# Performance work log

Measured on AMD Instinct MI355X. Metric: run time of the kernel, lower is better.

Reference implementation:

```python
import jax, jax.numpy as jnp
import numpy as np

D_MODEL = 128
N_HEADS = 4
D_K = D_V = 32
LN_EPS = 1e-5


def setup_inputs() -> dict:
    key = jax.random.key(0)
    ks = jax.random.split(key, 12)
    B, S = 8, 2048
    scale = 1.0 / np.sqrt(D_MODEL)
    inp = {
        "Q": jax.random.normal(ks[0], (B, S, D_MODEL), jnp.float32),
        "K": jax.random.normal(ks[1], (B, S, D_MODEL), jnp.float32),
        "V": jax.random.normal(ks[2], (B, S, D_MODEL), jnp.float32),
        "attn_mask": jnp.zeros((B, S, S), jnp.bool_),
        # learned params (torch Linear stored as [in, out] so y = x @ W + b)
        "wq": jax.random.normal(ks[3], (D_MODEL, N_HEADS * D_K), jnp.float32) * scale,
        "bq": jnp.zeros((N_HEADS * D_K,), jnp.float32),
        "wk": jax.random.normal(ks[4], (D_MODEL, N_HEADS * D_K), jnp.float32) * scale,
        "bk": jnp.zeros((N_HEADS * D_K,), jnp.float32),
        "wv": jax.random.normal(ks[5], (D_MODEL, N_HEADS * D_V), jnp.float32) * scale,
        "bv": jnp.zeros((N_HEADS * D_V,), jnp.float32),
        "wo": jax.random.normal(ks[6], (N_HEADS * D_V, D_MODEL), jnp.float32) * scale,
        "bo": jnp.zeros((D_MODEL,), jnp.float32),
        "gamma": jnp.ones((D_MODEL,), jnp.float32),
        "beta": jnp.zeros((D_MODEL,), jnp.float32),
    }
    return inp


def _layer_norm(x, gamma, beta):
    mu = jnp.mean(x, axis=-1, keepdims=True)
    var = jnp.mean(jnp.square(x - mu), axis=-1, keepdims=True)
    return (x - mu) * jax.lax.rsqrt(var + LN_EPS) * gamma + beta


def reference(Q, K, V, attn_mask, wq, bq, wk, bk, wv, bv, wo, bo, gamma, beta):
    B, S, _ = Q.shape
    residual = Q
    # project and split heads: [B, H, S, Dk]
    q = (Q @ wq + bq).reshape(B, S, N_HEADS, D_K).transpose(0, 2, 1, 3)
    k = (K @ wk + bk).reshape(B, S, N_HEADS, D_K).transpose(0, 2, 1, 3)
    v = (V @ wv + bv).reshape(B, S, N_HEADS, D_V).transpose(0, 2, 1, 3)
    scores = jnp.einsum("bhqd,bhkd->bhqk", q, k) / np.sqrt(D_K)
    scores = jnp.where(attn_mask[:, None, :, :], -1e9, scores)
    attn = jax.nn.softmax(scores, axis=-1)
    context = jnp.einsum("bhqk,bhkd->bhqd", attn, v)
    context = context.transpose(0, 2, 1, 3).reshape(B, S, N_HEADS * D_V)
    output = context @ wo + bo
    out = _layer_norm(output + residual, gamma, beta)
    return out, attn
```

## Files before the change

kernel.cpp:

```cpp
#include <hip/hip_runtime.h>

typedef _Float16 f16;
typedef __attribute__((ext_vector_type(8))) _Float16 f16x8;
typedef __attribute__((ext_vector_type(4))) _Float16 f16x4;
typedef __attribute__((ext_vector_type(2))) __fp16 fp16x2;
typedef __attribute__((ext_vector_type(4))) float f32x4;
typedef unsigned int u32;
typedef __attribute__((ext_vector_type(2))) unsigned int u32x2;
typedef __attribute__((ext_vector_type(4))) unsigned int u32x4;

#define S_LEN 2048
#define NB 8
#define NH 4
#define DM 128
#define DK 32

static __device__ __forceinline__ f32x4 mfma_16x16x32(f16x8 a, f16x8 b, f32x4 c) {
  return __builtin_amdgcn_mfma_f32_16x16x32_f16(a, b, c, 0, 0, 0);
}
static __device__ __forceinline__ float exp2f_fast(float x) {
  return __builtin_amdgcn_exp2f(x);
}

union H8 { f16x8 v; fp16x2 h[4]; };
union H4 { f16x4 v; fp16x2 h[2]; };

__global__ __launch_bounds__(256) void pack_mask_kernel(
    const unsigned char* __restrict__ mask, u32* __restrict__ words)
{
  const int tid = blockIdx.x * 256 + threadIdx.x;
  u32x4 v = *(const u32x4*)(mask + (size_t)tid * 16);
  u32 bits = 0;
#pragma unroll
  for (int i = 0; i < 4; ++i) {
    u32 u = v[i];
#pragma unroll
    for (int k = 0; k < 4; ++k)
      bits |= (((u >> (8 * k)) & 0xffu) ? 1u : 0u) << (4 * i + k);
  }
  u32 other = __shfl_xor(bits, 1);
  if ((threadIdx.x & 1) == 0) words[tid >> 1] = bits | (other << 16);
}

__global__ __launch_bounds__(256) void proj_kernel(
    const float* __restrict__ Qx, const float* __restrict__ Kx, const float* __restrict__ Vx,
    const float* __restrict__ wq, const float* __restrict__ bq,
    const float* __restrict__ wk, const float* __restrict__ bk,
    const float* __restrict__ wv, const float* __restrict__ bv,
    f16* __restrict__ qh, f16* __restrict__ kh, f16* __restrict__ vt)
{
  const int mode = blockIdx.y;
  const float* X = (mode == 0) ? Qx : (mode == 1) ? Kx : Vx;
  const float* W = (mode == 0) ? wq : (mode == 1) ? wk : wv;
  const float* Bp = (mode == 0) ? bq : (mode == 1) ? bk : bv;

  __shared__ f16 wl[128 * 136];
#pragma unroll
  for (int i = 0; i < 16; ++i) {
    int idx = (i * 256 + threadIdx.x) * 4;
    int k = idx >> 7, j = idx & 127;
    f32x4 w4 = *(const f32x4*)(W + idx);
    wl[(j    ) * 136 + k] = (f16)w4[0];
    wl[(j + 1) * 136 + k] = (f16)w4[1];
    wl[(j + 2) * 136 + k] = (f16)w4[2];
    wl[(j + 3) * 136 + k] = (f16)w4[3];
  }
  __syncthreads();

  const int wave = threadIdx.x >> 6, lane = threadIdx.x & 63;
  const int ln = lane & 15, hi = lane >> 4;
  const int rows0 = blockIdx.x * 64 + wave * 16;
  const int b = rows0 >> 11;
  const int s0 = rows0 & (S_LEN - 1);

  f32x4 acc[8];
#pragma unroll
  for (int jg = 0; jg < 8; ++jg) acc[jg] = (f32x4){0.f, 0.f, 0.f, 0.f};

#pragma unroll
  for (int kc = 0; kc < 4; ++kc) {
    const float* xp = X + (size_t)(rows0 + ln) * DM + kc * 32 + hi * 8;
    f32x4 x0 = *(const f32x4*)xp;
    f32x4 x1 = *(const f32x4*)(xp + 4);
    H8 hx;
    hx.h[0] = __builtin_amdgcn_cvt_pkrtz(x0[0], x0[1]);
    hx.h[1] = __builtin_amdgcn_cvt_pkrtz(x0[2], x0[3]);
    hx.h[2] = __builtin_amdgcn_cvt_pkrtz(x1[0], x1[1]);
    hx.h[3] = __builtin_amdgcn_cvt_pkrtz(x1[2], x1[3]);
    const f16* wp = wl + ln * 136 + kc * 32 + hi * 8;
    if (mode < 2) {
#pragma unroll
      for (int jg = 0; jg < 8; ++jg) {
        f16x8 wf = *(const f16x8*)(wp + jg * 2176);
        acc[jg] = mfma_16x16x32(wf, hx.v, acc[jg]);
      }
    } else {
#pragma unroll
      for (int jg = 0; jg < 8; ++jg) {
        f16x8 wf = *(const f16x8*)(wp + jg * 2176);
        acc[jg] = mfma_16x16x32(hx.v, wf, acc[jg]);
      }
    }
  }

  if (mode < 2) {
    const float sc = (mode == 0) ? 0.25503531f : 1.0f;
    f16* outp = (mode == 0) ? qh : kh;
    const int s = s0 + ln;
#pragma unroll
    for (int jg = 0; jg < 8; ++jg) {
      int j0 = jg * 16 + hi * 4;
      f32x4 bb = *(const f32x4*)(Bp + j0);
      int h = jg >> 1;
      int dd0 = (jg & 1) * 16 + hi * 4;
      f16x4 e;
#pragma unroll
      for (int r = 0; r < 4; ++r) e[r] = (f16)((acc[jg][r] + bb[r]) * sc);
      *(f16x4*)(outp + ((size_t)(b * NH + h) * S_LEN + s) * DK + dd0) = e;
    }
  } else {
    const int t4 = s0 >> 5;
    const int halfq = (s0 >> 4) & 1;
#pragma unroll
    for (int jt = 0; jt < 8; ++jt) {
      int h = jt >> 1;
      int dv = (jt & 1) * 16 + ln;
      float bb = Bp[jt * 16 + ln];
      H4 u;
      u.h[0] = __builtin_amdgcn_cvt_pkrtz(acc[jt][0] + bb, acc[jt][1] + bb);
      u.h[1] = __builtin_amdgcn_cvt_pkrtz(acc[jt][2] + bb, acc[jt][3] + bb);
      f16* dst = vt + (size_t)(b * NH + h) * DK * S_LEN + t4 * 1024 + dv * 32 + hi * 8 + halfq * 4;
      *(f16x4*)dst = u.v;
    }
  }
}

__global__ __launch_bounds__(256, 4) void attn_kernel(
    const f16* __restrict__ qh, const f16* __restrict__ kh, const f16* __restrict__ vt,
    const u32* __restrict__ words,
    float* __restrict__ attn, float* __restrict__ ctx)
{
  const int bx = blockIdx.x;
  const int bh = bx >> 5;
  const int qp = bx & 31;
  const int wave = threadIdx.x >> 6;
  const int tile = wave >> 1;
  const int half = wave & 1;
  const int lane = threadIdx.x & 63;
  const int ln = lane & 15, hi = lane >> 4;
  const int b = bh >> 2, h = bh & 3;
  const int base = qp * 64 + tile * 32;
  const int rA = base + ln;
  const int rB = rA + 16;
  const int kv0 = half * (S_LEN / 2);

  __shared__ f32x4 pt[4][2][16][16];
  __shared__ float sums[2][2][2][16];

  const f16* kbase = kh + (size_t)bh * S_LEN * DK;
  const f16* vbase = vt + (size_t)bh * DK * S_LEN;
  const u32* wrA = words + ((size_t)b * S_LEN + rA) * (S_LEN / 32);
  const u32* wrB = words + ((size_t)b * S_LEN + rB) * (S_LEN / 32);

  const f16x8 qA = *(const f16x8*)(qh + ((size_t)bh * S_LEN + rA) * DK + hi * 8);
  const f16x8 qB = *(const f16x8*)(qh + ((size_t)bh * S_LEN + rB) * DK + hi * 8);
  const f32x4 zero = {0.f, 0.f, 0.f, 0.f};

  float smA = 0.f, smB = 0.f;
  {
    const f16* kp = kbase + (size_t)(kv0 + ln) * DK + hi * 8;
    const u32* mpA = wrA + (kv0 >> 5);
    const u32* mpB = wrB + (kv0 >> 5);
    f16x8 k0 = *(const f16x8*)(kp);
    f16x8 k1 = *(const f16x8*)(kp + 512);
    f16x8 k2 = *(const f16x8*)(kp + 1024);
    f16x8 k3 = *(const f16x8*)(kp + 1536);
    u32x2 mA = *(const u32x2*)mpA;
    u32x2 mB = *(const u32x2*)mpB;
    for (int it = 0; it < 16; ++it) {
      f16x8 n0, n1, n2, n3;
      u32x2 nA, nB;
      if (it < 15) {
        n0 = *(const f16x8*)(kp + 2048);
        n1 = *(const f16x8*)(kp + 2560);
        n2 = *(const f16x8*)(kp + 3072);
        n3 = *(const f16x8*)(kp + 3584);
        nA = *(const u32x2*)(mpA + 2);
        nB = *(const u32x2*)(mpB + 2);
      }
      f32x4 sA0 = mfma_16x16x32(k0, qA, zero);
      f32x4 sA1 = mfma_16x16x32(k1, qA, zero);
      f32x4 sA2 = mfma_16x16x32(k2, qA, zero);
      f32x4 sA3 = mfma_16x16x32(k3, qA, zero);
      f32x4 sB0 = mfma_16x16x32(k0, qB, zero);
      f32x4 sB1 = mfma_16x16x32(k1, qB, zero);
      f32x4 sB2 = mfma_16x16x32(k2, qB, zero);
      f32x4 sB3 = mfma_16x16x32(k3, qB, zero);
      if (__any(((mA[0] | mA[1]) | (mB[0] | mB[1])) != 0u)) {
#pragma unroll
        for (int r = 0; r < 4; ++r) {
          float a0 = ((mA[0] >> (4 * hi + r)) & 1) ? 0.f : exp2f_fast(sA0[r]);
          float a1 = ((mA[0] >> (16 + 4 * hi + r)) & 1) ? 0.f : exp2f_fast(sA1[r]);
          float a2 = ((mA[1] >> (4 * hi + r)) & 1) ? 0.f : exp2f_fast(sA2[r]);
          float a3 = ((mA[1] >> (16 + 4 * hi + r)) & 1) ? 0.f : exp2f_fast(sA3[r]);
          smA += (a0 + a1) + (a2 + a3);
          float b0 = ((mB[0] >> (4 * hi + r)) & 1) ? 0.f : exp2f_fast(sB0[r]);
          float b1 = ((mB[0] >> (16 + 4 * hi + r)) & 1) ? 0.f : exp2f_fast(sB1[r]);
          float b2 = ((mB[1] >> (4 * hi + r)) & 1) ? 0.f : exp2f_fast(sB2[r]);
          float b3 = ((mB[1] >> (16 + 4 * hi + r)) & 1) ? 0.f : exp2f_fast(sB3[r]);
          smB += (b0 + b1) + (b2 + b3);
        }
      } else {
#pragma unroll
        for (int r = 0; r < 4; ++r) {
          smA += (exp2f_fast(sA0[r]) + exp2f_fast(sA1[r])) + (exp2f_fast(sA2[r]) + exp2f_fast(sA3[r]));
          smB += (exp2f_fast(sB0[r]) + exp2f_fast(sB1[r])) + (exp2f_fast(sB2[r]) + exp2f_fast(sB3[r]));
        }
      }
      k0 = n0; k1 = n1; k2 = n2; k3 = n3;
      mA = nA; mB = nB;
      kp += 2048; mpA += 2; mpB += 2;
    }
  }
  smA += __shfl_xor(smA, 16); smA += __shfl_xor(smA, 32);
  smB += __shfl_xor(smB, 16); smB += __shfl_xor(smB, 32);
  if (lane < 16) { sums[tile][half][0][ln] = smA; sums[tile][half][1][ln] = smB; }
  __syncthreads();
  const float linvA = -__builtin_amdgcn_logf(sums[tile][0][0][ln] + sums[tile][1][0][ln]);
  const float linvB = -__builtin_amdgcn_logf(sums[tile][0][1][ln] + sums[tile][1][1][ln]);

  f32x4 cA0 = zero, cA1 = zero, cB0 = zero, cB1 = zero;
  {
    const f16* kp = kbase + (size_t)(kv0 + ln) * DK + hi * 8;
    const f16* vp = vbase + (size_t)(kv0 >> 5) * 1024 + ln * 32 + hi * 8;
    const u32* mpA = wrA + (kv0 >> 5);
    const u32* mpB = wrB + (kv0 >> 5);
    float* dstA = attn + ((size_t)bh * S_LEN + base) * S_LEN + kv0;
    float* dstB = dstA + (size_t)16 * S_LEN;
    f16x8 k0 = *(const f16x8*)(kp);
    f16x8 k1 = *(const f16x8*)(kp + 512);
    f16x8 k2 = *(const f16x8*)(kp + 1024);
    f16x8 k3 = *(const f16x8*)(kp + 1536);
    for (int it = 0; it < 16; ++it) {
      f16x8 v0 = *(const f16x8*)(vp);
      f16x8 v1 = *(const f16x8*)(vp + 512);
      f16x8 v2 = *(const f16x8*)(vp + 1024);
      f16x8 v3 = *(const f16x8*)(vp + 1536);
      f16x8 n0, n1, n2, n3;
      if (it < 15) {
        n0 = *(const f16x8*)(kp + 2048);
        n1 = *(const f16x8*)(kp + 2560);
        n2 = *(const f16x8*)(kp + 3072);
        n3 = *(const f16x8*)(kp + 3584);
      }
      u32x2 mA = *(const u32x2*)mpA;
      u32x2 mB = *(const u32x2*)mpB;

      {
        f32x4 s0 = mfma_16x16x32(k0, qA, zero);
        f32x4 s1 = mfma_16x16x32(k1, qA, zero);
        f32x4 s2 = mfma_16x16x32(k2, qA, zero);
        f32x4 s3 = mfma_16x16x32(k3, qA, zero);
        f32x4 p0, p1, p2, p3;
        if (__any((mA[0] | mA[1]) != 0u)) {
#pragma unroll
          for (int r = 0; r < 4; ++r) {
            p0[r] = ((mA[0] >> (4 * hi + r)) & 1) ? 0.f : exp2f_fast(s0[r] + linvA);
            p1[r] = ((mA[0] >> (16 + 4 * hi + r)) & 1) ? 0.f : exp2f_fast(s1[r] + linvA);
            p2[r] = ((mA[1] >> (4 * hi + r)) & 1) ? 0.f : exp2f_fast(s2[r] + linvA);
            p3[r] = ((mA[1] >> (16 + 4 * hi + r)) & 1) ? 0.f : exp2f_fast(s3[r] + linvA);
          }
        } else {
#pragma unroll
          for (int r = 0; r < 4; ++r) {
            p0[r] = exp2f_fast(s0[r] + linvA);
            p1[r] = exp2f_fast(s1[r] + linvA);
            p2[r] = exp2f_fast(s2[r] + linvA);
            p3[r] = exp2f_fast(s3[r] + linvA);
          }
        }
        pt[wave][0][ln][(0 + hi) ^ (ln & 7)] = p0;
        pt[wave][0][ln][(4 + hi) ^ (ln & 7)] = p1;
        pt[wave][0][ln][(8 + hi) ^ (ln & 7)] = p2;
        pt[wave][0][ln][(12 + hi) ^ (ln & 7)] = p3;
        H8 ua, ub;
        ua.h[0] = __builtin_amdgcn_cvt_pkrtz(p0[0], p0[1]);
        ua.h[1] = __builtin_amdgcn_cvt_pkrtz(p0[2], p0[3]);
        ua.h[2] = __builtin_amdgcn_cvt_pkrtz(p1[0], p1[1]);
        ua.h[3] = __builtin_amdgcn_cvt_pkrtz(p1[2], p1[3]);
        ub.h[0] = __builtin_amdgcn_cvt_pkrtz(p2[0], p2[1]);
        ub.h[1] = __builtin_amdgcn_cvt_pkrtz(p2[2], p2[3]);
        ub.h[2] = __builtin_amdgcn_cvt_pkrtz(p3[0], p3[1]);
        ub.h[3] = __builtin_amdgcn_cvt_pkrtz(p3[2], p3[3]);
        cA0 = mfma_16x16x32(v0, ua.v, cA0);
        cA1 = mfma_16x16x32(v1, ua.v, cA1);
        cA0 = mfma_16x16x32(v2, ub.v, cA0);
        cA1 = mfma_16x16x32(v3, ub.v, cA1);
#pragma unroll
        for (int s4 = 0; s4 < 4; ++s4) {
          int row = s4 * 4 + hi;
          f32x4 val = pt[wave][0][row][ln ^ (row & 7)];
          __builtin_nontemporal_store(val, (f32x4*)(dstA + (size_t)row * S_LEN + ln * 4));
        }
      }
      {
        f32x4 s0 = mfma_16x16x32(k0, qB, zero);
        f32x4 s1 = mfma_16x16x32(k1, qB, zero);
        f32x4 s2 = mfma_16x16x32(k2, qB, zero);
        f32x4 s3 = mfma_16x16x32(k3, qB, zero);
        f32x4 p0, p1, p2, p3;
        if (__any((mB[0] | mB[1]) != 0u)) {
#pragma unroll
          for (int r = 0; r < 4; ++r) {
            p0[r] = ((mB[0] >> (4 * hi + r)) & 1) ? 0.f : exp2f_fast(s0[r] + linvB);
            p1[r] = ((mB[0] >> (16 + 4 * hi + r)) & 1) ? 0.f : exp2f_fast(s1[r] + linvB);
            p2[r] = ((mB[1] >> (4 * hi + r)) & 1) ? 0.f : exp2f_fast(s2[r] + linvB);
            p3[r] = ((mB[1] >> (16 + 4 * hi + r)) & 1) ? 0.f : exp2f_fast(s3[r] + linvB);
          }
        } else {
#pragma unroll
          for (int r = 0; r < 4; ++r) {
            p0[r] = exp2f_fast(s0[r] + linvB);
            p1[r] = exp2f_fast(s1[r] + linvB);
            p2[r] = exp2f_fast(s2[r] + linvB);
            p3[r] = exp2f_fast(s3[r] + linvB);
          }
        }
        pt[wave][1][ln][(0 + hi) ^ (ln & 7)] = p0;
        pt[wave][1][ln][(4 + hi) ^ (ln & 7)] = p1;
        pt[wave][1][ln][(8 + hi) ^ (ln & 7)] = p2;
        pt[wave][1][ln][(12 + hi) ^ (ln & 7)] = p3;
        H8 ua, ub;
        ua.h[0] = __builtin_amdgcn_cvt_pkrtz(p0[0], p0[1]);
        ua.h[1] = __builtin_amdgcn_cvt_pkrtz(p0[2], p0[3]);
        ua.h[2] = __builtin_amdgcn_cvt_pkrtz(p1[0], p1[1]);
        ua.h[3] = __builtin_amdgcn_cvt_pkrtz(p1[2], p1[3]);
        ub.h[0] = __builtin_amdgcn_cvt_pkrtz(p2[0], p2[1]);
        ub.h[1] = __builtin_amdgcn_cvt_pkrtz(p2[2], p2[3]);
        ub.h[2] = __builtin_amdgcn_cvt_pkrtz(p3[0], p3[1]);
        ub.h[3] = __builtin_amdgcn_cvt_pkrtz(p3[2], p3[3]);
        cB0 = mfma_16x16x32(v0, ua.v, cB0);
        cB1 = mfma_16x16x32(v1, ua.v, cB1);
        cB0 = mfma_16x16x32(v2, ub.v, cB0);
        cB1 = mfma_16x16x32(v3, ub.v, cB1);
#pragma unroll
        for (int s4 = 0; s4 < 4; ++s4) {
          int row = s4 * 4 + hi;
          f32x4 val = pt[wave][1][row][ln ^ (row & 7)];
          __builtin_nontemporal_store(val, (f32x4*)(dstB + (size_t)row * S_LEN + ln * 4));
        }
      }
      k0 = n0; k1 = n1; k2 = n2; k3 = n3;
      kp += 2048; vp += 2048; mpA += 2; mpB += 2;
      dstA += 64; dstB += 64;
    }
  }

  if (half == 1) {
    float* cb = (float*)&pt[tile * 2 + 1][0][0][0];
#pragma unroll
    for (int r = 0; r < 4; ++r) {
      cb[ln * 32 + hi * 4 + r] = cA0[r];
      cb[ln * 32 + 16 + hi * 4 + r] = cA1[r];
      cb[(16 + ln) * 32 + hi * 4 + r] = cB0[r];
      cb[(16 + ln) * 32 + 16 + hi * 4 + r] = cB1[r];
    }
  }
  __syncthreads();
  if (half == 0) {
    const float* cb = (const float*)&pt[tile * 2 + 1][0][0][0];
#pragma unroll
    for (int r = 0; r < 4; ++r) {
      cA0[r] += cb[ln * 32 + hi * 4 + r];
      cA1[r] += cb[ln * 32 + 16 + hi * 4 + r];
      cB0[r] += cb[(16 + ln) * 32 + hi * 4 + r];
      cB1[r] += cb[(16 + ln) * 32 + 16 + hi * 4 + r];
    }
    float* crowA = ctx + ((size_t)b * S_LEN + rA) * DM + h * DK;
    float* crowB = ctx + ((size_t)b * S_LEN + rB) * DM + h * DK;
    *(f32x4*)(crowA + hi * 4) = cA0;
    *(f32x4*)(crowA + 16 + hi * 4) = cA1;
    *(f32x4*)(crowB + hi * 4) = cB0;
    *(f32x4*)(crowB + 16 + hi * 4) = cB1;
  }
}

__global__ __launch_bounds__(256) void out_ln_kernel(
    const float* __restrict__ ctx, const float* __restrict__ Qin,
    const float* __restrict__ wo, const float* __restrict__ bo,
    const float* __restrict__ gamma, const float* __restrict__ beta,
    float* __restrict__ out)
{
  __shared__ f16 wl[128 * 136];
#pragma unroll
  for (int i = 0; i < 16; ++i) {
    int idx = (i * 256 + threadIdx.x) * 4;
    int k = idx >> 7, j = idx & 127;
    f32x4 w4 = *(const f32x4*)(wo + idx);
    wl[(j    ) * 136 + k] = (f16)w4[0];
    wl[(j + 1) * 136 + k] = (f16)w4[1];
    wl[(j + 2) * 136 + k] = (f16)w4[2];
    wl[(j + 3) * 136 + k] = (f16)w4[3];
  }
  __syncthreads();

  const int wave = threadIdx.x >> 6, lane = threadIdx.x & 63;
  const int ln = lane & 15, hi = lane >> 4;
  const int srow = blockIdx.x * 64 + wave * 16 + ln;

  f32x4 acc[8];
#pragma unroll
  for (int jg = 0; jg < 8; ++jg) acc[jg] = (f32x4){0.f, 0.f, 0.f, 0.f};

#pragma unroll
  for (int kc = 0; kc < 4; ++kc) {
    const float* xp = ctx + (size_t)srow * DM + kc * 32 + hi * 8;
    f32x4 x0 = *(const f32x4*)xp;
    f32x4 x1 = *(const f32x4*)(xp + 4);
    H8 hx;
    hx.h[0] = __builtin_amdgcn_cvt_pkrtz(x0[0], x0[1]);
    hx.h[1] = __builtin_amdgcn_cvt_pkrtz(x0[2], x0[3]);
    hx.h[2] = __builtin_amdgcn_cvt_pkrtz(x1[0], x1[1]);
    hx.h[3] = __builtin_amdgcn_cvt_pkrtz(x1[2], x1[3]);
    const f16* wp = wl + ln * 136 + kc * 32 + hi * 8;
#pragma unroll
    for (int jg = 0; jg < 8; ++jg) {
      f16x8 wf = *(const f16x8*)(wp + jg * 2176);
      acc[jg] = mfma_16x16x32(wf, hx.v, acc[jg]);
    }
  }

  float sm = 0.f, sq = 0.f;
#pragma unroll
  for (int jg = 0; jg < 8; ++jg) {
    int j0 = jg * 16 + hi * 4;
    f32x4 bb = *(const f32x4*)(bo + j0);
    f32x4 qq = *(const f32x4*)(Qin + (size_t)srow * DM + j0);
#pragma unroll
    for (int r = 0; r < 4; ++r) {
      float y = acc[jg][r] + bb[r] + qq[r];
      acc[jg][r] = y;
      sm += y; sq += y * y;
    }
  }
  sm += __shfl_xor(sm, 16); sm += __shfl_xor(sm, 32);
  sq += __shfl_xor(sq, 16); sq += __shfl_xor(sq, 32);
  const float mu = sm * (1.f / 128.f);
  const float var = sq * (1.f / 128.f) - mu * mu;
  const float rstd = rsqrtf(var + 1e-5f);
#pragma unroll
  for (int jg = 0; jg < 8; ++jg) {
    int j0 = jg * 16 + hi * 4;
    f32x4 g = *(const f32x4*)(gamma + j0);
    f32x4 be = *(const f32x4*)(beta + j0);
    f32x4 o;
#pragma unroll
    for (int r = 0; r < 4; ++r) o[r] = (acc[jg][r] - mu) * rstd * g[r] + be[r];
    *(f32x4*)(out + (size_t)srow * DM + j0) = o;
  }
}

extern "C" void kernel_launch(void* const* d_in, const int* in_sizes, int n_in,
                              void* d_out, int out_size, void* d_ws, size_t ws_size,
                              hipStream_t stream) {
  const float* Q    = (const float*)d_in[0];
  const float* K    = (const float*)d_in[1];
  const float* V    = (const float*)d_in[2];
  const unsigned char* mask = (const unsigned char*)d_in[3];
  const float* wq   = (const float*)d_in[4];
  const float* bq   = (const float*)d_in[5];
  const float* wk   = (const float*)d_in[6];
  const float* bk   = (const float*)d_in[7];
  const float* wv   = (const float*)d_in[8];
  const float* bv   = (const float*)d_in[9];
  const float* wo   = (const float*)d_in[10];
  const float* bo   = (const float*)d_in[11];
  const float* gamma= (const float*)d_in[12];
  const float* beta = (const float*)d_in[13];

  const size_t HEAD_ELEMS = (size_t)NB * NH * S_LEN * DK;

  f16* qh = (f16*)d_ws;
  f16* kh = qh + HEAD_ELEMS;
  f16* vt = kh + HEAD_ELEMS;
  float* ctx = (float*)(vt + HEAD_ELEMS);
  u32* words = (u32*)(ctx + (size_t)NB * S_LEN * DM);

  float* out  = (float*)d_out;
  float* attn = out + (size_t)NB * S_LEN * DM;

  pack_mask_kernel<<<8192, 256, 0, stream>>>(mask, words);
  proj_kernel<<<dim3(256, 3), 256, 0, stream>>>(Q, K, V, wq, bq, wk, bk, wv, bv, qh, kh, vt);
  attn_kernel<<<1024, 256, 0, stream>>>(qh, kh, vt, words, attn, ctx);
  out_ln_kernel<<<256, 256, 0, stream>>>(ctx, Q, wo, bo, gamma, beta, out);
}
```

Before: 193.3 us.

## Pre-transpose weights once, load MFMA fragments from global, store attn probs directly

A new small kernel converts all four weight matrices to f16 and transposes them once into workspace. The projection and output kernels then load weight fragments straight from global memory with register prefetching, instead of each block rebuilding a transposed copy in LDS. In the attention kernel, probability tiles are written straight from registers with nontemporal stores rather than staged through an LDS transpose. This gives each lane short 16-byte row segments, so global write coalescing is worse in exchange for fewer LDS round trips.

```diff
diff --git a/kernel.cpp b/kernel.cpp
--- a/kernel.cpp
+++ b/kernel.cpp
@@ -42,30 +42,48 @@
   if ((threadIdx.x & 1) == 0) words[tid >> 1] = bits | (other << 16);
 }
 
-__global__ __launch_bounds__(256) void proj_kernel(
+__global__ __launch_bounds__(256) void wtrans_kernel(
+    const float* __restrict__ wq, const float* __restrict__ wk,
+    const float* __restrict__ wv, const float* __restrict__ wo,
+    f16* __restrict__ wt)
+{
+  const float* W = (blockIdx.x == 0) ? wq : (blockIdx.x == 1) ? wk
+                 : (blockIdx.x == 2) ? wv : wo;
+  f16* dst = wt + (size_t)blockIdx.x * 16384;
+  __shared__ f16 tile[128 * 130];
+  const int t = threadIdx.x;
+#pragma unroll
+  for (int i = 0; i < 16; ++i) {
+    int idx = (i * 256 + t) * 4;
+    f32x4 w4 = *(const f32x4*)(W + idx);
+    int k = idx >> 7, j = idx & 127;
+    tile[(j    ) * 130 + k] = (f16)w4[0];
+    tile[(j + 1) * 130 + k] = (f16)w4[1];
+    tile[(j + 2) * 130 + k] = (f16)w4[2];
+    tile[(j + 3) * 130 + k] = (f16)w4[3];
+  }
+  __syncthreads();
+#pragma unroll
+  for (int i = 0; i < 8; ++i) {
+    int lin = (i * 256 + t) * 8;
+    int j = lin >> 7, k = lin & 127;
+    f16x8 v;
+#pragma unroll
+    for (int r = 0; r < 8; ++r) v[r] = tile[j * 130 + k + r];
+    *(f16x8*)(dst + lin) = v;
+  }
+}
+
+__global__ __launch_bounds__(256, 2) void proj_kernel(
     const float* __restrict__ Qx, const float* __restrict__ Kx, const float* __restrict__ Vx,
-    const float* __restrict__ wq, const float* __restrict__ bq,
-    const float* __restrict__ wk, const float* __restrict__ bk,
-    const float* __restrict__ wv, const float* __restrict__ bv,
+    const f16* __restrict__ wt,
+    const float* __restrict__ bq, const float* __restrict__ bk, const float* __restrict__ bv,
     f16* __restrict__ qh, f16* __restrict__ kh, f16* __restrict__ vt)
 {
   const int mode = blockIdx.y;
   const float* X = (mode == 0) ? Qx : (mode == 1) ? Kx : Vx;
-  const float* W = (mode == 0) ? wq : (mode == 1) ? wk : wv;
+  const f16* wm = wt + (size_t)mode * 16384;
   const float* Bp = (mode == 0) ? bq : (mode == 1) ? bk : bv;
-
-  __shared__ f16 wl[128 * 136];
-#pragma unroll
-  for (int i = 0; i < 16; ++i) {
-    int idx = (i * 256 + threadIdx.x) * 4;
-    int k = idx >> 7, j = idx & 127;
-    f32x4 w4 = *(const f32x4*)(W + idx);
-    wl[(j    ) * 136 + k] = (f16)w4[0];
-    wl[(j + 1) * 136 + k] = (f16)w4[1];
-    wl[(j + 2) * 136 + k] = (f16)w4[2];
-    wl[(j + 3) * 136 + k] = (f16)w4[3];
-  }
-  __syncthreads();
 
   const int wave = threadIdx.x >> 6, lane = threadIdx.x & 63;
   const int ln = lane & 15, hi = lane >> 4;
@@ -73,34 +91,43 @@
   const int b = rows0 >> 11;
   const int s0 = rows0 & (S_LEN - 1);
 
+  const float* xp = X + (size_t)(rows0 + ln) * DM + hi * 8;
+  H8 hx[4];
+#pragma unroll
+  for (int kc = 0; kc < 4; ++kc) {
+    f32x4 x0 = *(const f32x4*)(xp + kc * 32);
+    f32x4 x1 = *(const f32x4*)(xp + kc * 32 + 4);
+    hx[kc].h[0] = __builtin_amdgcn_cvt_pkrtz(x0[0], x0[1]);
+    hx[kc].h[1] = __builtin_amdgcn_cvt_pkrtz(x0[2], x0[3]);
+    hx[kc].h[2] = __builtin_amdgcn_cvt_pkrtz(x1[0], x1[1]);
+    hx[kc].h[3] = __builtin_amdgcn_cvt_pkrtz(x1[2], x1[3]);
+  }
+
   f32x4 acc[8];
 #pragma unroll
   for (int jg = 0; jg < 8; ++jg) acc[jg] = (f32x4){0.f, 0.f, 0.f, 0.f};
 
+  const f16* wp = wm + ln * 128 + hi * 8;
+  f16x8 wf[8];
+#pragma unroll
+  for (int jg = 0; jg < 8; ++jg) wf[jg] = *(const f16x8*)(wp + jg * 2048);
 #pragma unroll
   for (int kc = 0; kc < 4; ++kc) {
-    const float* xp = X + (size_t)(rows0 + ln) * DM + kc * 32 + hi * 8;
-    f32x4 x0 = *(const f32x4*)xp;
-    f32x4 x1 = *(const f32x4*)(xp + 4);
-    H8 hx;
-    hx.h[0] = __builtin_amdgcn_cvt_pkrtz(x0[0], x0[1]);
-    hx.h[1] = __builtin_amdgcn_cvt_pkrtz(x0[2], x0[3]);
-    hx.h[2] = __builtin_amdgcn_cvt_pkrtz(x1[0], x1[1]);
-    hx.h[3] = __builtin_amdgcn_cvt_pkrtz(x1[2], x1[3]);
-    const f16* wp = wl + ln * 136 + kc * 32 + hi * 8;
+    f16x8 nwf[8];
+    if (kc < 3) {
+#pragma unroll
+      for (int jg = 0; jg < 8; ++jg)
+        nwf[jg] = *(const f16x8*)(wp + jg * 2048 + (kc + 1) * 32);
+    }
     if (mode < 2) {
 #pragma unroll
-      for (int jg = 0; jg < 8; ++jg) {
-        f16x8 wf = *(const f16x8*)(wp + jg * 2176);
-        acc[jg] = mfma_16x16x32(wf, hx.v, acc[jg]);
-      }
+      for (int jg = 0; jg < 8; ++jg) acc[jg] = mfma_16x16x32(wf[jg], hx[kc].v, acc[jg]);
     } else {
 #pragma unroll
-      for (int jg = 0; jg < 8; ++jg) {
-        f16x8 wf = *(const f16x8*)(wp + jg * 2176);
-        acc[jg] = mfma_16x16x32(hx.v, wf, acc[jg]);
-      }
-    }
+      for (int jg = 0; jg < 8; ++jg) acc[jg] = mfma_16x16x32(hx[kc].v, wf[jg], acc[jg]);
+    }
+#pragma unroll
+    for (int jg = 0; jg < 8; ++jg) wf[jg] = nwf[jg];
   }
 
   if (mode < 2) {
@@ -154,7 +181,7 @@
   const int rB = rA + 16;
   const int kv0 = half * (S_LEN / 2);
 
-  __shared__ f32x4 pt[4][2][16][16];
+  __shared__ float ctxbuf[2][32][32];
   __shared__ float sums[2][2][2][16];
 
   const f16* kbase = kh + (size_t)bh * S_LEN * DK;
@@ -235,8 +262,8 @@
     const f16* vp = vbase + (size_t)(kv0 >> 5) * 1024 + ln * 32 + hi * 8;
     const u32* mpA = wrA + (kv0 >> 5);
     const u32* mpB = wrB + (kv0 >> 5);
-    float* dstA = attn + ((size_t)bh * S_LEN + base) * S_LEN + kv0;
-    float* dstB = dstA + (size_t)16 * S_LEN;
+    float* rowA = attn + ((size_t)bh * S_LEN + rA) * S_LEN + kv0 + 4 * hi;
+    float* rowB = attn + ((size_t)bh * S_LEN + rB) * S_LEN + kv0 + 4 * hi;
     f16x8 k0 = *(const f16x8*)(kp);
     f16x8 k1 = *(const f16x8*)(kp + 512);
     f16x8 k2 = *(const f16x8*)(kp + 1024);
@@ -279,10 +306,10 @@
             p3[r] = exp2f_fast(s3[r] + linvA);
           }
         }
-        pt[wave][0][ln][(0 + hi) ^ (ln & 7)] = p0;
-        pt[wave][0][ln][(4 + hi) ^ (ln & 7)] = p1;
-        pt[wave][0][ln][(8 + hi) ^ (ln & 7)] = p2;
-        pt[wave][0][ln][(12 + hi) ^ (ln & 7)] = p3;
+        __builtin_nontemporal_store(p0, (f32x4*)(rowA));
+        __builtin_nontemporal_store(p1, (f32x4*)(rowA + 16));
+        __builtin_nontemporal_store(p2, (f32x4*)(rowA + 32));
+        __builtin_nontemporal_store(p3, (f32x4*)(rowA + 48));
         H8 ua, ub;
         ua.h[0] = __builtin_amdgcn_cvt_pkrtz(p0[0], p0[1]);
         ua.h[1] = __builtin_amdgcn_cvt_pkrtz(p0[2], p0[3]);
@@ -296,12 +323,6 @@
         cA1 = mfma_16x16x32(v1, ua.v, cA1);
         cA0 = mfma_16x16x32(v2, ub.v, cA0);
         cA1 = mfma_16x16x32(v3, ub.v, cA1);
-#pragma unroll
-        for (int s4 = 0; s4 < 4; ++s4) {
-          int row = s4 * 4 + hi;
-          f32x4 val = pt[wave][0][row][ln ^ (row & 7)];
-          __builtin_nontemporal_store(val, (f32x4*)(dstA + (size_t)row * S_LEN + ln * 4));
-        }
       }
       {
         f32x4 s0 = mfma_16x16x32(k0, qB, zero);
@@ -326,10 +347,10 @@
             p3[r] = exp2f_fast(s3[r] + linvB);
           }
         }
-        pt[wave][1][ln][(0 + hi) ^ (ln & 7)] = p0;
-        pt[wave][1][ln][(4 + hi) ^ (ln & 7)] = p1;
-        pt[wave][1][ln][(8 + hi) ^ (ln & 7)] = p2;
-        pt[wave][1][ln][(12 + hi) ^ (ln & 7)] = p3;
+        __builtin_nontemporal_store(p0, (f32x4*)(rowB));
+        __builtin_nontemporal_store(p1, (f32x4*)(rowB + 16));
+        __builtin_nontemporal_store(p2, (f32x4*)(rowB + 32));
+        __builtin_nontemporal_store(p3, (f32x4*)(rowB + 48));
         H8 ua, ub;
         ua.h[0] = __builtin_amdgcn_cvt_pkrtz(p0[0], p0[1]);
         ua.h[1] = __builtin_amdgcn_cvt_pkrtz(p0[2], p0[3]);
@@ -343,21 +364,15 @@
         cB1 = mfma_16x16x32(v1, ua.v, cB1);
         cB0 = mfma_16x16x32(v2, ub.v, cB0);
         cB1 = mfma_16x16x32(v3, ub.v, cB1);
-#pragma unroll
-        for (int s4 = 0; s4 < 4; ++s4) {
-          int row = s4 * 4 + hi;
-          f32x4 val = pt[wave][1][row][ln ^ (row & 7)];
-          __builtin_nontemporal_store(val, (f32x4*)(dstB + (size_t)row * S_LEN + ln * 4));
-        }
       }
       k0 = n0; k1 = n1; k2 = n2; k3 = n3;
       kp += 2048; vp += 2048; mpA += 2; mpB += 2;
-      dstA += 64; dstB += 64;
+      rowA += 64; rowB += 64;
     }
   }
 
   if (half == 1) {
-    float* cb = (float*)&pt[tile * 2 + 1][0][0][0];
+    float* cb = (float*)&ctxbuf[tile][0][0];
 #pragma unroll
     for (int r = 0; r < 4; ++r) {
       cb[ln * 32 + hi * 4 + r] = cA0[r];
@@ -368,7 +383,7 @@
   }
   __syncthreads();
   if (half == 0) {
-    const float* cb = (const float*)&pt[tile * 2 + 1][0][0][0];
+    const float* cb = (const float*)&ctxbuf[tile][0][0];
 #pragma unroll
     for (int r = 0; r < 4; ++r) {
       cA0[r] += cb[ln * 32 + hi * 4 + r];
@@ -385,49 +400,50 @@
   }
 }
 
-__global__ __launch_bounds__(256) void out_ln_kernel(
+__global__ __launch_bounds__(256, 2) void out_ln_kernel(
     const float* __restrict__ ctx, const float* __restrict__ Qin,
-    const float* __restrict__ wo, const float* __restrict__ bo,
+    const f16* __restrict__ wt,
+    const float* __restrict__ bo,
     const float* __restrict__ gamma, const float* __restrict__ beta,
     float* __restrict__ out)
 {
-  __shared__ f16 wl[128 * 136];
-#pragma unroll
-  for (int i = 0; i < 16; ++i) {
-    int idx = (i * 256 + threadIdx.x) * 4;
-    int k = idx >> 7, j = idx & 127;
-    f32x4 w4 = *(const f32x4*)(wo + idx);
-    wl[(j    ) * 136 + k] = (f16)w4[0];
-    wl[(j + 1) * 136 + k] = (f16)w4[1];
-    wl[(j + 2) * 136 + k] = (f16)w4[2];
-    wl[(j + 3) * 136 + k] = (f16)w4[3];
-  }
-  __syncthreads();
-
+  const f16* wm = wt + (size_t)3 * 16384;
   const int wave = threadIdx.x >> 6, lane = threadIdx.x & 63;
   const int ln = lane & 15, hi = lane >> 4;
   const int srow = blockIdx.x * 64 + wave * 16 + ln;
 
+  const float* xp = ctx + (size_t)srow * DM + hi * 8;
+  H8 hx[4];
+#pragma unroll
+  for (int kc = 0; kc < 4; ++kc) {
+    f32x4 x0 = *(const f32x4*)(xp + kc * 32);
+    f32x4 x1 = *(const f32x4*)(xp + kc * 32 + 4);
+    hx[kc].h[0] = __builtin_amdgcn_cvt_pkrtz(x0[0], x0[1]);
+    hx[kc].h[1] = __builtin_amdgcn_cvt_pkrtz(x0[2], x0[3]);
+    hx[kc].h[2] = __builtin_amdgcn_cvt_pkrtz(x1[0], x1[1]);
+    hx[kc].h[3] = __builtin_amdgcn_cvt_pkrtz(x1[2], x1[3]);
+  }
+
   f32x4 acc[8];
 #pragma unroll
   for (int jg = 0; jg < 8; ++jg) acc[jg] = (f32x4){0.f, 0.f, 0.f, 0.f};
 
+  const f16* wp = wm + ln * 128 + hi * 8;
+  f16x8 wf[8];
+#pragma unroll
+  for (int jg = 0; jg < 8; ++jg) wf[jg] = *(const f16x8*)(wp + jg * 2048);
 #pragma unroll
   for (int kc = 0; kc < 4; ++kc) {
-    const float* xp = ctx + (size_t)srow * DM + kc * 32 + hi * 8;
-    f32x4 x0 = *(const f32x4*)xp;
-    f32x4 x1 = *(const f32x4*)(xp + 4);
-    H8 hx;
-    hx.h[0] = __builtin_amdgcn_cvt_pkrtz(x0[0], x0[1]);
-    hx.h[1] = __builtin_amdgcn_cvt_pkrtz(x0[2], x0[3]);
-    hx.h[2] = __builtin_amdgcn_cvt_pkrtz(x1[0], x1[1]);
-    hx.h[3] = __builtin_amdgcn_cvt_pkrtz(x1[2], x1[3]);
-    const f16* wp = wl + ln * 136 + kc * 32 + hi * 8;
-#pragma unroll
-    for (int jg = 0; jg < 8; ++jg) {
-      f16x8 wf = *(const f16x8*)(wp + jg * 2176);
-      acc[jg] = mfma_16x16x32(wf, hx.v, acc[jg]);
-    }
+    f16x8 nwf[8];
+    if (kc < 3) {
+#pragma unroll
+      for (int jg = 0; jg < 8; ++jg)
+        nwf[jg] = *(const f16x8*)(wp + jg * 2048 + (kc + 1) * 32);
+    }
+#pragma unroll
+    for (int jg = 0; jg < 8; ++jg) acc[jg] = mfma_16x16x32(wf[jg], hx[kc].v, acc[jg]);
+#pragma unroll
+    for (int jg = 0; jg < 8; ++jg) wf[jg] = nwf[jg];
   }
 
   float sm = 0.f, sq = 0.f;
@@ -485,12 +501,14 @@
   f16* vt = kh + HEAD_ELEMS;
   float* ctx = (float*)(vt + HEAD_ELEMS);
   u32* words = (u32*)(ctx + (size_t)NB * S_LEN * DM);
+  f16* wt = (f16*)(words + (size_t)NB * S_LEN * (S_LEN / 32));
 
   float* out  = (float*)d_out;
   float* attn = out + (size_t)NB * S_LEN * DM;
 
   pack_mask_kernel<<<8192, 256, 0, stream>>>(mask, words);
-  proj_kernel<<<dim3(256, 3), 256, 0, stream>>>(Q, K, V, wq, bq, wk, bk, wv, bv, qh, kh, vt);
+  wtrans_kernel<<<4, 256, 0, stream>>>(wq, wk, wv, wo, wt);
+  proj_kernel<<<dim3(256, 3), 256, 0, stream>>>(Q, K, V, wt, bq, bk, bv, qh, kh, vt);
   attn_kernel<<<1024, 256, 0, stream>>>(qh, kh, vt, words, attn, ctx);
-  out_ln_kernel<<<256, 256, 0, stream>>>(ctx, Q, wo, bo, gamma, beta, out);
-}
+  out_ln_kernel<<<256, 256, 0, stream>>>(ctx, Q, wt, bo, gamma, beta, out);
+}
```

After: 205.5 us. 1.06x slower.
